# Optimization experiments

Measured on AMD Instinct MI355X. Metric: run time of the kernel, lower is better.

## Reference

```python
import jax, jax.numpy as jnp
import numpy as np

T, H, HS, NH = 1024, 2048, 64, 32
TM, TD = 32, 64  # time-mix / time-decay LoRA dims for hidden_size != 4096


def _layernorm(x, w, b, eps=1e-5):
    mu = jnp.mean(x, axis=-1, keepdims=True)
    var = jnp.mean(jnp.square(x - mu), axis=-1, keepdims=True)
    return (x - mu) * jax.lax.rsqrt(var + eps) * w + b


def setup_inputs() -> dict:
    key = jax.random.key(0)
    ks = jax.random.split(key, 16)
    s = 0.02
    return {
        'x': jax.random.normal(ks[0], (1, T, H), jnp.float32),
        'state1': jax.random.normal(ks[1], (1, H), jnp.float32),
        'state2': jax.random.normal(ks[2], (NH, HS, HS), jnp.float32) * s,
        'ln1_w': jnp.ones((H,), jnp.float32),
        'ln1_b': jnp.zeros((H,), jnp.float32),
        'time_maa_x': jax.random.normal(ks[3], (1, 1, H), jnp.float32) * s,
        'time_maa': jax.random.normal(ks[4], (5, 1, H), jnp.float32) * s,
        'time_maa_w1': jax.random.normal(ks[5], (H, 5 * TM), jnp.float32) * s,
        'time_maa_w2': jax.random.normal(ks[6], (5, TM, H), jnp.float32) * s,
        'time_decay_w1': jax.random.normal(ks[7], (H, TD), jnp.float32) * s,
        'time_decay_w2': jax.random.normal(ks[8], (TD, H), jnp.float32) * s,
        'time_decay_p': jax.random.normal(ks[9], (NH, 1, HS), jnp.float32),
        'time_first': jax.random.normal(ks[10], (NH, 1, HS), jnp.float32) * s,
        'W_r': jax.random.normal(ks[11], (H, H), jnp.float32) * s,
        'W_k': jax.random.normal(ks[12], (H, H), jnp.float32) * s,
        'W_v': jax.random.normal(ks[13], (H, H), jnp.float32) * s,
        'W_g': jax.random.normal(ks[14], (H, H), jnp.float32) * s,
        'W_o': jax.random.normal(ks[15], (H, H), jnp.float32) * s,
        'ln_x_w': jnp.ones((H,), jnp.float32),
        'ln_x_b': jnp.zeros((H,), jnp.float32),
    }


def _forward(x, state1, state2, ln1_w, ln1_b, time_maa_x, time_maa,
             time_maa_w1, time_maa_w2, time_decay_w1, time_decay_w2,
             time_decay_p, time_first, W_r, W_k, W_v, W_g, W_o, ln_x_w, ln_x_b):
    last_x = x
    xl = _layernorm(x, ln1_w, ln1_b)                 # (1,T,H)
    Tn = xl.shape[1]
    # token shift: sx = shift(x) - x, with state1 as the t=-1 token
    past = jnp.concatenate([state1[:, None, :], xl[:, :-1, :]], axis=1)
    sx = past - xl                                    # (1,T,H)
    state1_out = xl[:, -1, :]
    # data-dependent time-mix (LoRA through w1/w2)
    xxx = xl + sx * time_maa_x                        # (1,T,H)
    t5 = jnp.tanh(xxx[0] @ time_maa_w1)               # (T,5*TM)
    t5 = t5.reshape(Tn, 5, TM).transpose(1, 0, 2)     # (5,T,TM)
    mix = jnp.einsum('ftm,fmh->fth', t5, time_maa_w2) # (5,T,H)
    x5 = xl + sx * (mix + time_maa)                   # (5,T,H)
    mw, mk, mv, mr, mg = x5[0], x5[1], x5[2], x5[3], x5[4]
    r = (mr @ W_r).reshape(Tn, NH, HS)
    k = (mk @ W_k).reshape(Tn, NH, HS)
    v = (mv @ W_v).reshape(Tn, NH, HS)
    g = jax.nn.silu(mg @ W_g)                         # (T,H)
    # data-dependent decay
    td = (jnp.tanh(mw @ time_decay_w1) @ time_decay_w2).reshape(Tn, NH, 1, HS)
    td = td + time_decay_p                            # (T,NH,1,HS)
    td = jnp.exp(-jnp.exp(jnp.clip(td, -9.72, 2.27)))
    # WKV linear-attention recurrence
    kv = jnp.einsum('thi,thj->thij', v, k)            # (T,NH,HS,HS)

    def step(s2, inp):
        kv_t, r_t, td_t = inp
        tmp = kv_t * time_first + s2                  # (NH,HS,HS)
        wkv_t = jnp.einsum('hij,hj->hi', tmp, r_t)    # (NH,HS)
        return kv_t + s2 * td_t, wkv_t

    state2_out, wkv = jax.lax.scan(step, state2, (kv, r, td))  # wkv (T,NH,HS)
    # group-norm over head dim, then affine with ln_x params at hidden width
    y = _layernorm(wkv, 1.0, 0.0).reshape(1, Tn, H)
    y = (y * ln_x_w + ln_x_b) * g[None]
    y = y @ W_o
    return last_x + y, state1_out, state2_out


def reference(x, state1, state2, ln1_w, ln1_b, time_maa_x, time_maa,
              time_maa_w1, time_maa_w2, time_decay_w1, time_decay_w2,
              time_decay_p, time_first, W_r, W_k, W_v, W_g, W_o, ln_x_w, ln_x_b):
    return _forward(x, state1, state2, ln1_w, ln1_b, time_maa_x, time_maa,
                    time_maa_w1, time_maa_w2, time_decay_w1, time_decay_w2,
                    time_decay_p, time_first, W_r, W_k, W_v, W_g, W_o, ln_x_w, ln_x_b)
```

## Files before the change

kernel.cpp:

```cpp
#include <hip/hip_runtime.h>
#include <hip/hip_bf16.h>
#include <math.h>

#define TLEN 1024
#define HDIM 2048
#define NHEAD 32
#define HSZ 64
#define THE (TLEN * HDIM)
#define NC 32
#define CT (TLEN / NC)

typedef __attribute__((ext_vector_type(8))) short bf16x8;
typedef __attribute__((ext_vector_type(4))) float f32x4;

__device__ __forceinline__ float waveRedSum(float v) {
#pragma unroll
  for (int off = 32; off > 0; off >>= 1) v += __shfl_xor(v, off, 64);
  return v;
}

__device__ __forceinline__ void gll16(const __hip_bfloat16* g, __hip_bfloat16* l) {
  __builtin_amdgcn_global_load_lds(
      (const __attribute__((address_space(1))) void*)g,
      (__attribute__((address_space(3))) void*)l, 16, 0, 0);
}

struct TrArgs {
  const float* src[8];
  __hip_bfloat16* dst[8];
  int R[8];
  int C[8];
};

__global__ __launch_bounds__(256) void transp_kernel(TrArgs ta) {
  const int z = blockIdx.z;
  const int R = ta.R[z], C = ta.C[z];
  const int c0 = blockIdx.x * 32, r0 = blockIdx.y * 32;
  if (c0 >= C || r0 >= R) return;
  __shared__ float tile[32][33];
  const int tx = threadIdx.x & 31, ty = threadIdx.x >> 5;
  const float* src = ta.src[z];
  __hip_bfloat16* dst = ta.dst[z];
#pragma unroll
  for (int i = 0; i < 4; i++)
    tile[ty + i * 8][tx] = src[(size_t)(r0 + ty + i * 8) * C + c0 + tx];
  __syncthreads();
#pragma unroll
  for (int i = 0; i < 4; i++)
    dst[(size_t)(c0 + ty + i * 8) * R + r0 + tx] = __float2bfloat16(tile[tx][ty + i * 8]);
}

__global__ __launch_bounds__(256) void ln1_kernel(const float* __restrict__ x,
                                                  const float* __restrict__ w,
                                                  const float* __restrict__ b,
                                                  float* __restrict__ xl,
                                                  float* __restrict__ s1out) {
  const int t = blockIdx.x;
  const int tid = threadIdx.x;
  const int wid = tid >> 6, lane = tid & 63;
  const float4* xr = (const float4*)(x + (size_t)t * HDIM);
  float4 a = xr[tid];
  float4 c = xr[tid + 256];
  float va[8] = {a.x, a.y, a.z, a.w, c.x, c.y, c.z, c.w};
  float sum = 0.f;
#pragma unroll
  for (int i = 0; i < 8; i++) sum += va[i];
  sum = waveRedSum(sum);
  __shared__ float red[8];
  if (lane == 0) red[wid] = sum;
  __syncthreads();
  const float mu = (red[0] + red[1] + red[2] + red[3]) * (1.f / HDIM);
  float vs = 0.f;
#pragma unroll
  for (int i = 0; i < 8; i++) { float d = va[i] - mu; vs += d * d; }
  vs = waveRedSum(vs);
  if (lane == 0) red[4 + wid] = vs;
  __syncthreads();
  const float rstd = rsqrtf((red[4] + red[5] + red[6] + red[7]) * (1.f / HDIM) + 1e-5f);
  float* xrow = xl + (size_t)t * HDIM;
#pragma unroll
  for (int i = 0; i < 8; i++) {
    const int idx = (i < 4) ? (4 * tid + i) : (1024 + 4 * tid + (i - 4));
    const float o = (va[i] - mu) * rstd * w[idx] + b[idx];
    xrow[idx] = o;
    if (t == TLEN - 1) s1out[idx] = o;
  }
}

__global__ __launch_bounds__(256) void tokshift_kernel(const float* __restrict__ xl,
                                                       const float* __restrict__ s1,
                                                       const float* __restrict__ tmx,
                                                       __hip_bfloat16* __restrict__ xxx) {
  const int t = blockIdx.x;
  const int h = blockIdx.y * 256 + threadIdx.x;
  const float cur = xl[(size_t)t * HDIM + h];
  const float past = (t > 0) ? xl[(size_t)(t - 1) * HDIM + h] : s1[h];
  xxx[(size_t)t * HDIM + h] = __float2bfloat16(cur + (past - cur) * tmx[h]);
}

__global__ __launch_bounds__(256) void mix_kernel(const float* __restrict__ t5,
                                                  const float* __restrict__ xl,
                                                  const float* __restrict__ s1,
                                                  const float* __restrict__ w2,
                                                  const float* __restrict__ maa,
                                                  __hip_bfloat16* __restrict__ x5b) {
  const int h = blockIdx.x * 256 + threadIdx.x;
  const int t0 = blockIdx.y * 8;
  __shared__ float t5L[8 * 160];
  for (int i = threadIdx.x; i < 8 * 160; i += 256) {
    const int rr = i / 160, cc = i - rr * 160;
    t5L[i] = t5[(size_t)(t0 + rr) * 160 + cc];
  }
  __syncthreads();
  float mixv[8][5];
#pragma unroll
  for (int ts = 0; ts < 8; ts++)
#pragma unroll
    for (int f = 0; f < 5; f++) mixv[ts][f] = 0.f;
#pragma unroll
  for (int f = 0; f < 5; f++) {
#pragma unroll 4
    for (int m = 0; m < 32; m++) {
      const float w2v = w2[(size_t)(f * 32 + m) * HDIM + h];
#pragma unroll
      for (int ts = 0; ts < 8; ts++) mixv[ts][f] += t5L[ts * 160 + f * 32 + m] * w2v;
    }
  }
#pragma unroll
  for (int ts = 0; ts < 8; ts++) {
    const int t = t0 + ts;
    const float cur = xl[(size_t)t * HDIM + h];
    const float past = (t > 0) ? xl[(size_t)(t - 1) * HDIM + h] : s1[h];
    const float sx = past - cur;
#pragma unroll
    for (int f = 0; f < 5; f++) {
      const float v = cur + sx * (mixv[ts][f] + maa[(size_t)f * HDIM + h]);
      x5b[(size_t)f * THE + (size_t)t * HDIM + h] = __float2bfloat16(v);
    }
  }
}

struct GemmArgs {
  const __hip_bfloat16* A[8];
  const __hip_bfloat16* B[8];
  void* C[8];
  const float* aux[8];
  int epi[8];
  int M, N, K, Ks;
};

__global__ __launch_bounds__(256) void gemm_bt(GemmArgs ga) {
  const int z = blockIdx.z;
  const __hip_bfloat16* __restrict__ A = ga.A[z];
  const __hip_bfloat16* __restrict__ Bt = ga.B[z];
  const int N = ga.N, K = ga.K, Ks = ga.Ks;
  const int epi = ga.epi[z];
  const float* __restrict__ aux = ga.aux[z];
  void* Cz = ga.C[z];

  __shared__ __align__(16) __hip_bfloat16 As[2][128 * 64];
  __shared__ __align__(16) __hip_bfloat16 Bs[2][128 * 64];

  const int tid = threadIdx.x;
  const int wid = tid >> 6;
  const int lane = tid & 63;

  int bx = blockIdx.x, by = blockIdx.y;
  if (gridDim.x == 8 && gridDim.y == 16) {
    const int flat = bx + 8 * by;
    const int xcd = flat & 7, rem = flat >> 3;
    bx = rem & 7;
    by = xcd + 8 * (rem >> 3);
  }
  const int m0 = bx * 128;
  const int n0 = by * 128;
  const int wr = wid >> 1, wc = wid & 1;

  const int srow = lane >> 3;
  const int chunkS = (lane & 7) ^ srow;
  const __hip_bfloat16* aSrcQ[4];
  const __hip_bfloat16* bSrcQ[4];
#pragma unroll
  for (int q = 0; q < 4; q++) {
    const int arow = wid * 32 + q * 8 + srow;
    int brow = n0 + arow; if (brow > N - 1) brow = N - 1;
    aSrcQ[q] = A + (size_t)(m0 + arow) * Ks + chunkS * 8;
    bSrcQ[q] = Bt + (size_t)brow * Ks + chunkS * 8;
  }

  f32x4 acc[4][4];
#pragma unroll
  for (int m = 0; m < 4; m++)
#pragma unroll
    for (int n = 0; n < 4; n++) acc[m][n] = 0.f;

  const int lr = lane & 15;
  const int cbase = lane >> 4;
  int aoffk[2], boffk[2];
#pragma unroll
  for (int kg = 0; kg < 2; kg++) {
    const int phys = (kg * 4 + cbase) ^ (lr & 7);
    aoffk[kg] = (wr * 64 + lr) * 64 + phys * 8;
    boffk[kg] = (wc * 64 + lr) * 64 + phys * 8;
  }

#define STAGE(BUF, KT)                                              \
  do {                                                              \
    _Pragma("unroll") for (int q = 0; q < 4; q++) {                 \
      gll16(aSrcQ[q] + (KT), &As[BUF][(wid * 32 + q * 8) * 64]);    \
      gll16(bSrcQ[q] + (KT), &Bs[BUF][(wid * 32 + q * 8) * 64]);    \
    }                                                               \
  } while (0)

  STAGE(0, 0);
  int cur = 0;
  for (int kt = 0; kt < K; kt += 64) {
    const bool more = (kt + 64 < K);
    if (more) {
      STAGE(cur ^ 1, kt + 64);
      asm volatile("s_waitcnt vmcnt(8)" ::: "memory");
    } else {
      asm volatile("s_waitcnt vmcnt(0)" ::: "memory");
    }
    __builtin_amdgcn_s_barrier();
#pragma unroll
    for (int kg = 0; kg < 2; kg++) {
      bf16x8 af[4], bfv[4];
#pragma unroll
      for (int m = 0; m < 4; m++) af[m] = *(const bf16x8*)&As[cur][aoffk[kg] + m * 16 * 64];
#pragma unroll
      for (int n = 0; n < 4; n++) bfv[n] = *(const bf16x8*)&Bs[cur][boffk[kg] + n * 16 * 64];
#pragma unroll
      for (int m = 0; m < 4; m++)
#pragma unroll
        for (int n = 0; n < 4; n++)
          acc[m][n] = __builtin_amdgcn_mfma_f32_16x16x32_bf16(af[m], bfv[n], acc[m][n], 0, 0, 0);
    }
    __builtin_amdgcn_s_barrier();
    cur ^= 1;
  }
#undef STAGE

  const int r4 = (lane >> 4) * 4;
#pragma unroll
  for (int m = 0; m < 4; m++) {
#pragma unroll
    for (int n = 0; n < 4; n++) {
      const int gn = n0 + wc * 64 + n * 16 + lr;
      if (gn < N) {
#pragma unroll
        for (int r = 0; r < 4; r++) {
          const int gm = m0 + wr * 64 + m * 16 + r4 + r;
          const size_t idx = (size_t)gm * N + gn;
          const float v = acc[m][n][r];
          switch (epi) {
            case 0: ((__hip_bfloat16*)Cz)[idx] = __float2bfloat16(v); break;
            case 1: ((__hip_bfloat16*)Cz)[idx] = __float2bfloat16(v / (1.f + expf(-v))); break;
            case 2: ((float*)Cz)[idx] = tanhf(v); break;
            case 3: ((__hip_bfloat16*)Cz)[idx] = __float2bfloat16(tanhf(v)); break;
            case 5: ((float*)Cz)[idx] = v + aux[idx]; break;
            case 6: ((float*)Cz)[idx] = v; break;
          }
        }
      }
    }
  }
}

__global__ __launch_bounds__(256) void comb8_tanh_f32(const float* __restrict__ p,
                                                      float* __restrict__ o, int n) {
  const int i = blockIdx.x * 256 + threadIdx.x;
  float s = 0.f;
#pragma unroll
  for (int k = 0; k < 8; k++) s += p[(size_t)k * n + i];
  o[i] = tanhf(s);
}

__global__ __launch_bounds__(256) void comb8_tanh_bf16(const float* __restrict__ p,
                                                       __hip_bfloat16* __restrict__ o, int n) {
  const int i = blockIdx.x * 256 + threadIdx.x;
  float s = 0.f;
#pragma unroll
  for (int k = 0; k < 8; k++) s += p[(size_t)k * n + i];
  o[i] = __float2bfloat16(tanhf(s));
}

__global__ __launch_bounds__(256) void comb4_resid(const float* __restrict__ p,
                                                   const float* __restrict__ x,
                                                   float* __restrict__ o) {
  const int i = blockIdx.x * 256 + threadIdx.x;
  const float4 a = ((const float4*)p)[i];
  const float4 b = ((const float4*)(p + THE))[i];
  const float4 c = ((const float4*)(p + 2 * (size_t)THE))[i];
  const float4 d = ((const float4*)(p + 3 * (size_t)THE))[i];
  const float4 e = ((const float4*)x)[i];
  ((float4*)o)[i] = make_float4(a.x + b.x + c.x + d.x + e.x,
                                a.y + b.y + c.y + d.y + e.y,
                                a.z + b.z + c.z + d.z + e.z,
                                a.w + b.w + c.w + d.w + e.w);
}

__global__ __launch_bounds__(256) void tdcalc_kernel(const __hip_bfloat16* __restrict__ tw,
                                                     const __hip_bfloat16* __restrict__ dw2t,
                                                     const float* __restrict__ dp,
                                                     float* __restrict__ td) {
  const int t0 = blockIdx.x * 4;
  const int n = blockIdx.y * 256 + threadIdx.x;
  __shared__ float twL[4][64];
  {
    const int row = threadIdx.x >> 6, col = threadIdx.x & 63;
    twL[row][col] = __bfloat162float(tw[(size_t)(t0 + row) * 64 + col]);
  }
  __syncthreads();
  float acc[4] = {0.f, 0.f, 0.f, 0.f};
  const bf16x8* drow = (const bf16x8*)(dw2t + (size_t)n * 64);
#pragma unroll
  for (int ch = 0; ch < 8; ch++) {
    const bf16x8 v = drow[ch];
#pragma unroll
    for (int e = 0; e < 8; e++) {
      const float b = __builtin_bit_cast(float,
          (unsigned)((unsigned short)v[e]) << 16);
      const int col = ch * 8 + e;
#pragma unroll
      for (int r = 0; r < 4; r++) acc[r] = fmaf(twL[r][col], b, acc[r]);
    }
  }
  const float dpn = dp[n];
#pragma unroll
  for (int r = 0; r < 4; r++) {
    float wv = acc[r] + dpn;
    wv = fminf(fmaxf(wv, -9.72f), 2.27f);
    td[(size_t)(t0 + r) * HDIM + n] = expf(-expf(wv));
  }
}

__global__ __launch_bounds__(64) void decay_kernel(const __hip_bfloat16* __restrict__ rb,
                                                   const float* __restrict__ td,
                                                   __hip_bfloat16* __restrict__ rt,
                                                   float* __restrict__ Ptot) {
  const int blk = blockIdx.x;
  const int c = blk >> 5, h = blk & 31;
  const int j = threadIdx.x;
  const int hb = h * HSZ;
  const int t0 = c * CT;
  float A = 1.f;
  for (int t = 0; t < CT; t++) {
    const size_t rowb = (size_t)(t0 + t) * HDIM + hb;
    rt[(((size_t)c * NHEAD + h) * CT + t) * HSZ + j] =
        __float2bfloat16(__bfloat162float(rb[rowb + j]) * A);
    A *= td[rowb + j];
  }
  Ptot[((size_t)c * NHEAD + h) * HSZ + j] = A;
}

__global__ __launch_bounds__(256) void scan_local_kernel(const __hip_bfloat16* __restrict__ kb,
                                                         const __hip_bfloat16* __restrict__ rb,
                                                         const float* __restrict__ td,
                                                         const __hip_bfloat16* __restrict__ vb,
                                                         float* __restrict__ wkv,
                                                         float* __restrict__ qT) {
  const int blk = blockIdx.x;
  const int c = blk >> 5, h = blk & 31;
  const int w = threadIdx.x >> 6;
  const int i = threadIdx.x & 63;
  __shared__ float plds[2][4][64];

  float s[16];
#pragma unroll
  for (int q = 0; q < 16; q++) s[q] = 0.f;

  const int t0 = c * CT;
  const int hb = h * HSZ;

  for (int t = 0; t < CT; t++) {
    const size_t rowb = (size_t)(t0 + t) * HDIM + hb;
    const unsigned* kw = (const unsigned*)(kb + rowb + w * 16);
    const unsigned* rw = (const unsigned*)(rb + rowb + w * 16);
    const float* tdw = td + rowb + w * 16;
    const float vi = __bfloat162float(vb[rowb + i]);
    float p = 0.f;
#pragma unroll
    for (int m = 0; m < 8; m++) {
      const unsigned kpair = kw[m];
      const unsigned rpair = rw[m];
      const float k0 = __builtin_bit_cast(float, kpair << 16);
      const float k1 = __builtin_bit_cast(float, kpair & 0xffff0000u);
      const float r0 = __builtin_bit_cast(float, rpair << 16);
      const float r1 = __builtin_bit_cast(float, rpair & 0xffff0000u);
      const float td0 = tdw[2 * m];
      const float td1 = tdw[2 * m + 1];
      const float kv0 = vi * k0;
      const float kv1 = vi * k1;
      p = fmaf(r0, s[2 * m], p);
      p = fmaf(r1, s[2 * m + 1], p);
      s[2 * m] = fmaf(s[2 * m], td0, kv0);
      s[2 * m + 1] = fmaf(s[2 * m + 1], td1, kv1);
    }
    plds[t & 1][w][i] = p;
    __syncthreads();
    if (w == 0) {
      wkv[rowb + i] = plds[t & 1][0][i] + plds[t & 1][1][i] +
                      plds[t & 1][2][i] + plds[t & 1][3][i];
    }
  }
  float* qbase = qT + (((size_t)c * NHEAD + h) * HSZ + w * 16) * HSZ + i;
#pragma unroll
  for (int q = 0; q < 16; q++) qbase[(size_t)q * HSZ] = s[q];
}

__global__ __launch_bounds__(64) void scan_s_kernel(const float* __restrict__ qT,
                                                    const float* __restrict__ Ptot,
                                                    const float* __restrict__ s2in,
                                                    __hip_bfloat16* __restrict__ s0b,
                                                    float* __restrict__ s2out) {
  const int h = blockIdx.x, i = blockIdx.y, j = threadIdx.x;
  float s = s2in[((size_t)h * HSZ + i) * HSZ + j];
#pragma unroll 4
  for (int c = 0; c < NC; c++) {
    s0b[(((size_t)c * NHEAD + h) * HSZ + i) * HSZ + j] = __float2bfloat16(s);
    s = fmaf(s, Ptot[((size_t)c * NHEAD + h) * HSZ + j],
             qT[(((size_t)c * NHEAD + h) * HSZ + j) * HSZ + i]);
  }
  s2out[((size_t)h * HSZ + i) * HSZ + j] = s;
}

__global__ __launch_bounds__(256) void corr_kernel(const __hip_bfloat16* __restrict__ rt,
                                                   const __hip_bfloat16* __restrict__ s0b,
                                                   float* __restrict__ wkv) {
  const int c = blockIdx.x, h = blockIdx.y;
  const int w = threadIdx.x >> 6;
  const int lane = threadIdx.x & 63;
  const int lr = lane & 15, lk = (lane >> 4) * 8;
  const __hip_bfloat16* rbase = rt + (((size_t)c * NHEAD + h) * CT) * HSZ;
  const __hip_bfloat16* sbase = s0b + (((size_t)c * NHEAD + h) * HSZ) * HSZ;
  float* wbase = wkv + (size_t)(c * CT) * HDIM + h * HSZ;
#pragma unroll
  for (int mt = 0; mt < CT / 16; mt++) {
    f32x4 acc = {0.f, 0.f, 0.f, 0.f};
#pragma unroll
    for (int ks = 0; ks < 2; ks++) {
      bf16x8 af = *(const bf16x8*)(rbase + (size_t)(mt * 16 + lr) * HSZ + ks * 32 + lk);
      bf16x8 bf = *(const bf16x8*)(sbase + (size_t)(w * 16 + lr) * HSZ + ks * 32 + lk);
      acc = __builtin_amdgcn_mfma_f32_16x16x32_bf16(af, bf, acc, 0, 0, 0);
    }
    const int row = mt * 16 + (lane >> 4) * 4;
    const int col = w * 16 + lr;
#pragma unroll
    for (int r = 0; r < 4; r++)
      wbase[(size_t)(row + r) * HDIM + col] += acc[r];
  }
}

__global__ __launch_bounds__(256) void gnorm_kernel(const float* __restrict__ wkv,
                                                    const __hip_bfloat16* __restrict__ kb,
                                                    const __hip_bfloat16* __restrict__ rb,
                                                    const float* __restrict__ tf,
                                                    const __hip_bfloat16* __restrict__ vb,
                                                    const __hip_bfloat16* __restrict__ gb,
                                                    const float* __restrict__ lnw,
                                                    const float* __restrict__ lnb,
                                                    __hip_bfloat16* __restrict__ yA) {
  const int t = blockIdx.x;
  const int wid = threadIdx.x >> 6, j = threadIdx.x & 63;
  const int h = blockIdx.y * 4 + wid;
  const size_t idx = (size_t)t * HDIM + h * HSZ + j;
  const float kj = __bfloat162float(kb[idx]);
  const float rj = __bfloat162float(rb[idx]);
  const float dg = waveRedSum(rj * tf[h * HSZ + j] * kj);
  const float v = wkv[idx] + dg * __bfloat162float(vb[idx]);
  const float mu = waveRedSum(v) * (1.f / HSZ);
  const float d = v - mu;
  const float var = waveRedSum(d * d) * (1.f / HSZ);
  float y = d * rsqrtf(var + 1e-5f);
  y = y * lnw[h * HSZ + j] + lnb[h * HSZ + j];
  y *= __bfloat162float(gb[idx]);
  yA[idx] = __float2bfloat16(y);
}

extern "C" void kernel_launch(void* const* d_in, const int* in_sizes, int n_in,
                              void* d_out, int out_size, void* d_ws, size_t ws_size,
                              hipStream_t stream) {
  (void)in_sizes; (void)n_in; (void)out_size; (void)ws_size;

  const float* x    = (const float*)d_in[0];
  const float* s1   = (const float*)d_in[1];
  const float* s2   = (const float*)d_in[2];
  const float* ln1w = (const float*)d_in[3];
  const float* ln1b = (const float*)d_in[4];
  const float* tmx  = (const float*)d_in[5];
  const float* tmaa = (const float*)d_in[6];
  const float* w1   = (const float*)d_in[7];
  const float* w2   = (const float*)d_in[8];
  const float* dw1  = (const float*)d_in[9];
  const float* dw2  = (const float*)d_in[10];
  const float* dp   = (const float*)d_in[11];
  const float* tf   = (const float*)d_in[12];
  const float* Wr   = (const float*)d_in[13];
  const float* Wk   = (const float*)d_in[14];
  const float* Wv   = (const float*)d_in[15];
  const float* Wg   = (const float*)d_in[16];
  const float* Wo   = (const float*)d_in[17];
  const float* lnxw = (const float*)d_in[18];
  const float* lnxb = (const float*)d_in[19];

  float* out0  = (float*)d_out;
  float* s1out = out0 + (size_t)TLEN * HDIM;
  float* s2out = s1out + HDIM;

  char* wp = (char*)d_ws;
  size_t off = 0;
  auto carve = [&](size_t bytes) -> void* {
    void* r = wp + off;
    off += (bytes + 255) & ~(size_t)255;
    return r;
  };

  __hip_bfloat16* wrt  = (__hip_bfloat16*)carve((size_t)HDIM * HDIM * 2);
  __hip_bfloat16* wkt  = (__hip_bfloat16*)carve((size_t)HDIM * HDIM * 2);
  __hip_bfloat16* wvt  = (__hip_bfloat16*)carve((size_t)HDIM * HDIM * 2);
  __hip_bfloat16* wgt  = (__hip_bfloat16*)carve((size_t)HDIM * HDIM * 2);
  __hip_bfloat16* wot  = (__hip_bfloat16*)carve((size_t)HDIM * HDIM * 2);
  __hip_bfloat16* w1t  = (__hip_bfloat16*)carve((size_t)160 * HDIM * 2);
  __hip_bfloat16* dw1t = (__hip_bfloat16*)carve((size_t)64 * HDIM * 2);
  __hip_bfloat16* dw2t = (__hip_bfloat16*)carve((size_t)HDIM * 64 * 2);
  float* xl            = (float*)carve((size_t)THE * 4);
  __hip_bfloat16* xxx  = (__hip_bfloat16*)carve((size_t)THE * 2);
  float* t5            = (float*)carve((size_t)TLEN * 160 * 4);
  __hip_bfloat16* x5b  = (__hip_bfloat16*)carve((size_t)5 * THE * 2);
  __hip_bfloat16* rb   = (__hip_bfloat16*)carve((size_t)THE * 2);
  __hip_bfloat16* kb   = (__hip_bfloat16*)carve((size_t)THE * 2);
  __hip_bfloat16* vb   = (__hip_bfloat16*)carve((size_t)THE * 2);
  __hip_bfloat16* gb   = (__hip_bfloat16*)carve((size_t)THE * 2);
  __hip_bfloat16* tw   = (__hip_bfloat16*)carve((size_t)TLEN * 64 * 2);
  float* td            = (float*)carve((size_t)THE * 4);
  float* wkv           = (float*)carve((size_t)THE * 4);
  __hip_bfloat16* yA   = (__hip_bfloat16*)carve((size_t)THE * 2);

  float* qT            = (float*)x5b;
  __hip_bfloat16* rt   = (__hip_bfloat16*)xl;
  __hip_bfloat16* s0b  = (__hip_bfloat16*)td;
  float* Ptot          = (float*)t5;
  float* pg1           = (float*)td;
  float* pg4           = (float*)xxx;
  float* pg6           = (float*)x5b;

  TrArgs ta;
  const float* srcs[8] = {Wr, Wk, Wv, Wg, Wo, w1, dw1, dw2};
  __hip_bfloat16* dsts[8] = {wrt, wkt, wvt, wgt, wot, w1t, dw1t, dw2t};
  const int Rs[8] = {HDIM, HDIM, HDIM, HDIM, HDIM, HDIM, HDIM, 64};
  const int Cs[8] = {HDIM, HDIM, HDIM, HDIM, HDIM, 160, 64, HDIM};
  for (int z = 0; z < 8; z++) { ta.src[z] = srcs[z]; ta.dst[z] = dsts[z]; ta.R[z] = Rs[z]; ta.C[z] = Cs[z]; }
  transp_kernel<<<dim3(64, 64, 8), 256, 0, stream>>>(ta);

  ln1_kernel<<<dim3(TLEN), 256, 0, stream>>>(x, ln1w, ln1b, xl, s1out);

  tokshift_kernel<<<dim3(TLEN, HDIM / 256), 256, 0, stream>>>(xl, s1, tmx, xxx);

  {
    GemmArgs g{};
    for (int ks = 0; ks < 8; ks++) {
      g.A[ks] = xxx + ks * 256;
      g.B[ks] = w1t + ks * 256;
      g.C[ks] = pg1 + (size_t)ks * TLEN * 160;
      g.epi[ks] = 6;
    }
    g.M = TLEN; g.N = 160; g.K = 256; g.Ks = HDIM;
    gemm_bt<<<dim3(TLEN / 128, 2, 8), 256, 0, stream>>>(g);
    comb8_tanh_f32<<<dim3(TLEN * 160 / 256), 256, 0, stream>>>(pg1, t5, TLEN * 160);
  }

  mix_kernel<<<dim3(HDIM / 256, TLEN / 8), 256, 0, stream>>>(t5, xl, s1, w2, tmaa, x5b);

  {
    GemmArgs g{};
    g.A[0] = x5b + (size_t)3 * THE; g.B[0] = wrt; g.C[0] = rb; g.epi[0] = 0;
    g.A[1] = x5b + (size_t)1 * THE; g.B[1] = wkt; g.C[1] = kb; g.epi[1] = 0;
    g.A[2] = x5b + (size_t)2 * THE; g.B[2] = wvt; g.C[2] = vb; g.epi[2] = 0;
    g.A[3] = x5b + (size_t)4 * THE; g.B[3] = wgt; g.C[3] = gb; g.epi[3] = 1;
    g.M = TLEN; g.N = HDIM; g.K = HDIM; g.Ks = HDIM;
    gemm_bt<<<dim3(TLEN / 128, HDIM / 128, 4), 256, 0, stream>>>(g);
  }

  {
    GemmArgs g{};
    for (int ks = 0; ks < 8; ks++) {
      g.A[ks] = x5b + ks * 256;
      g.B[ks] = dw1t + ks * 256;
      g.C[ks] = pg4 + (size_t)ks * TLEN * 64;
      g.epi[ks] = 6;
    }
    g.M = TLEN; g.N = 64; g.K = 256; g.Ks = HDIM;
    gemm_bt<<<dim3(TLEN / 128, 1, 8), 256, 0, stream>>>(g);
    comb8_tanh_bf16<<<dim3(TLEN * 64 / 256), 256, 0, stream>>>(pg4, tw, TLEN * 64);
  }

  tdcalc_kernel<<<dim3(TLEN / 4, HDIM / 256), 256, 0, stream>>>(tw, dw2t, dp, td);

  decay_kernel<<<dim3(NC * NHEAD), 64, 0, stream>>>(rb, td, rt, Ptot);
  scan_local_kernel<<<dim3(NC * NHEAD), 256, 0, stream>>>(kb, rb, td, vb, wkv, qT);
  scan_s_kernel<<<dim3(NHEAD, HSZ), 64, 0, stream>>>(qT, Ptot, s2, s0b, s2out);
  corr_kernel<<<dim3(NC, NHEAD), 256, 0, stream>>>(rt, s0b, wkv);

  gnorm_kernel<<<dim3(TLEN, NHEAD / 4), 256, 0, stream>>>(wkv, kb, rb, tf, vb, gb, lnxw, lnxb, yA);

  {
    GemmArgs g{};
    for (int ks = 0; ks < 4; ks++) {
      g.A[ks] = yA + ks * 512;
      g.B[ks] = wot + ks * 512;
      g.C[ks] = pg6 + (size_t)ks * THE;
      g.epi[ks] = 6;
    }
    g.M = TLEN; g.N = HDIM; g.K = 512; g.Ks = HDIM;
    gemm_bt<<<dim3(TLEN / 128, HDIM / 128, 4), 256, 0, stream>>>(g);
    comb4_resid<<<dim3(THE / 4 / 256), 256, 0, stream>>>(pg6, x, out0);
  }
}
```

Measured before the change: 269.1 us.

## Fuse token-shift into LayerNorm, decay into local scan, and correction into group-norm

The token-shift kernel is removed: ln1 now normalizes both the current and previous row of x and writes the shifted bf16 mix directly. The decay-prefix kernel is folded into scan_local, which now also emits the decayed r values and the chunk's total decay. The MFMA correction kernel is replaced by a per-thread 64-element bf16 dot product inside gnorm. This cuts three launches and their intermediate round trips, at the cost of computing the previous row's LayerNorm twice and doing the correction with scalar FMAs instead of matrix instructions.

After: 312.9 us. 16.3% more time.

```diff
diff --git a/kernel.cpp b/kernel.cpp
--- a/kernel.cpp
+++ b/kernel.cpp
@@ -17,6 +17,10 @@
 #pragma unroll
   for (int off = 32; off > 0; off >>= 1) v += __shfl_xor(v, off, 64);
   return v;
+}
+
+__device__ __forceinline__ float bf2f(unsigned short u) {
+  return __builtin_bit_cast(float, (unsigned)u << 16);
 }
 
 __device__ __forceinline__ void gll16(const __hip_bfloat16* g, __hip_bfloat16* l) {
@@ -53,49 +57,54 @@
 __global__ __launch_bounds__(256) void ln1_kernel(const float* __restrict__ x,
                                                   const float* __restrict__ w,
                                                   const float* __restrict__ b,
+                                                  const float* __restrict__ s1,
+                                                  const float* __restrict__ tmx,
                                                   float* __restrict__ xl,
+                                                  __hip_bfloat16* __restrict__ xxx,
                                                   float* __restrict__ s1out) {
   const int t = blockIdx.x;
   const int tid = threadIdx.x;
   const int wid = tid >> 6, lane = tid & 63;
   const float4* xr = (const float4*)(x + (size_t)t * HDIM);
-  float4 a = xr[tid];
-  float4 c = xr[tid + 256];
+  const float4* xp = (const float4*)(x + (size_t)(t > 0 ? t - 1 : 0) * HDIM);
+  float4 a = xr[tid], c = xr[tid + 256];
+  float4 ap = xp[tid], cp = xp[tid + 256];
   float va[8] = {a.x, a.y, a.z, a.w, c.x, c.y, c.z, c.w};
-  float sum = 0.f;
-#pragma unroll
-  for (int i = 0; i < 8; i++) sum += va[i];
+  float vp[8] = {ap.x, ap.y, ap.z, ap.w, cp.x, cp.y, cp.z, cp.w};
+  float sum = 0.f, sump = 0.f;
+#pragma unroll
+  for (int i = 0; i < 8; i++) { sum += va[i]; sump += vp[i]; }
   sum = waveRedSum(sum);
-  __shared__ float red[8];
-  if (lane == 0) red[wid] = sum;
+  sump = waveRedSum(sump);
+  __shared__ float red[16];
+  if (lane == 0) { red[wid] = sum; red[8 + wid] = sump; }
   __syncthreads();
   const float mu = (red[0] + red[1] + red[2] + red[3]) * (1.f / HDIM);
-  float vs = 0.f;
-#pragma unroll
-  for (int i = 0; i < 8; i++) { float d = va[i] - mu; vs += d * d; }
+  const float mup = (red[8] + red[9] + red[10] + red[11]) * (1.f / HDIM);
+  float vs = 0.f, vsp = 0.f;
+#pragma unroll
+  for (int i = 0; i < 8; i++) {
+    float d = va[i] - mu; vs += d * d;
+    float dp = vp[i] - mup; vsp += dp * dp;
+  }
   vs = waveRedSum(vs);
-  if (lane == 0) red[4 + wid] = vs;
+  vsp = waveRedSum(vsp);
+  if (lane == 0) { red[4 + wid] = vs; red[12 + wid] = vsp; }
   __syncthreads();
   const float rstd = rsqrtf((red[4] + red[5] + red[6] + red[7]) * (1.f / HDIM) + 1e-5f);
+  const float rstdp = rsqrtf((red[12] + red[13] + red[14] + red[15]) * (1.f / HDIM) + 1e-5f);
   float* xrow = xl + (size_t)t * HDIM;
+  __hip_bfloat16* xxrow = xxx + (size_t)t * HDIM;
 #pragma unroll
   for (int i = 0; i < 8; i++) {
     const int idx = (i < 4) ? (4 * tid + i) : (1024 + 4 * tid + (i - 4));
-    const float o = (va[i] - mu) * rstd * w[idx] + b[idx];
-    xrow[idx] = o;
-    if (t == TLEN - 1) s1out[idx] = o;
-  }
-}
-
-__global__ __launch_bounds__(256) void tokshift_kernel(const float* __restrict__ xl,
-                                                       const float* __restrict__ s1,
-                                                       const float* __restrict__ tmx,
-                                                       __hip_bfloat16* __restrict__ xxx) {
-  const int t = blockIdx.x;
-  const int h = blockIdx.y * 256 + threadIdx.x;
-  const float cur = xl[(size_t)t * HDIM + h];
-  const float past = (t > 0) ? xl[(size_t)(t - 1) * HDIM + h] : s1[h];
-  xxx[(size_t)t * HDIM + h] = __float2bfloat16(cur + (past - cur) * tmx[h]);
+    const float wv = w[idx], bv = b[idx];
+    const float cur = (va[i] - mu) * rstd * wv + bv;
+    const float past = (t > 0) ? (vp[i] - mup) * rstdp * wv + bv : s1[idx];
+    xrow[idx] = cur;
+    xxrow[idx] = __float2bfloat16(cur + (past - cur) * tmx[idx]);
+    if (t == TLEN - 1) s1out[idx] = cur;
+  }
 }
 
 __global__ __launch_bounds__(256) void mix_kernel(const float* __restrict__ t5,
@@ -319,8 +328,7 @@
     const bf16x8 v = drow[ch];
 #pragma unroll
     for (int e = 0; e < 8; e++) {
-      const float b = __builtin_bit_cast(float,
-          (unsigned)((unsigned short)v[e]) << 16);
+      const float b = bf2f((unsigned short)v[e]);
       const int col = ch * 8 + e;
 #pragma unroll
       for (int r = 0; r < 4; r++) acc[r] = fmaf(twL[r][col], b, acc[r]);
@@ -333,25 +341,6 @@
     wv = fminf(fmaxf(wv, -9.72f), 2.27f);
     td[(size_t)(t0 + r) * HDIM + n] = expf(-expf(wv));
   }
-}
-
-__global__ __launch_bounds__(64) void decay_kernel(const __hip_bfloat16* __restrict__ rb,
-                                                   const float* __restrict__ td,
-                                                   __hip_bfloat16* __restrict__ rt,
-                                                   float* __restrict__ Ptot) {
-  const int blk = blockIdx.x;
-  const int c = blk >> 5, h = blk & 31;
-  const int j = threadIdx.x;
-  const int hb = h * HSZ;
-  const int t0 = c * CT;
-  float A = 1.f;
-  for (int t = 0; t < CT; t++) {
-    const size_t rowb = (size_t)(t0 + t) * HDIM + hb;
-    rt[(((size_t)c * NHEAD + h) * CT + t) * HSZ + j] =
-        __float2bfloat16(__bfloat162float(rb[rowb + j]) * A);
-    A *= td[rowb + j];
-  }
-  Ptot[((size_t)c * NHEAD + h) * HSZ + j] = A;
 }
 
 __global__ __launch_bounds__(256) void scan_local_kernel(const __hip_bfloat16* __restrict__ kb,
@@ -359,7 +348,9 @@
                                                          const float* __restrict__ td,
                                                          const __hip_bfloat16* __restrict__ vb,
                                                          float* __restrict__ wkv,
-                                                         float* __restrict__ qT) {
+                                                         float* __restrict__ qT,
+                                                         __hip_bfloat16* __restrict__ rt,
+                                                         float* __restrict__ Ptot) {
   const int blk = blockIdx.x;
   const int c = blk >> 5, h = blk & 31;
   const int w = threadIdx.x >> 6;
@@ -372,6 +363,9 @@
 
   const int t0 = c * CT;
   const int hb = h * HSZ;
+  const int jSelf = w * 16 + (i & 15);
+  float Aself = 1.f;
+  __hip_bfloat16* rtbase = rt + (((size_t)c * NHEAD + h) * CT) * HSZ + jSelf;
 
   for (int t = 0; t < CT; t++) {
     const size_t rowb = (size_t)(t0 + t) * HDIM + hb;
@@ -397,6 +391,10 @@
       s[2 * m] = fmaf(s[2 * m], td0, kv0);
       s[2 * m + 1] = fmaf(s[2 * m + 1], td1, kv1);
     }
+    const float rself = __bfloat162float(rb[rowb + jSelf]);
+    if (i < 16) rtbase[(size_t)t * HSZ] = __float2bfloat16(rself * Aself);
+    Aself *= td[rowb + jSelf];
+
     plds[t & 1][w][i] = p;
     __syncthreads();
     if (w == 0) {
@@ -404,6 +402,7 @@
                       plds[t & 1][2][i] + plds[t & 1][3][i];
     }
   }
+  if (i < 16) Ptot[((size_t)c * NHEAD + h) * HSZ + jSelf] = Aself;
   float* qbase = qT + (((size_t)c * NHEAD + h) * HSZ + w * 16) * HSZ + i;
 #pragma unroll
   for (int q = 0; q < 16; q++) qbase[(size_t)q * HSZ] = s[q];
@@ -425,39 +424,14 @@
   s2out[((size_t)h * HSZ + i) * HSZ + j] = s;
 }
 
-__global__ __launch_bounds__(256) void corr_kernel(const __hip_bfloat16* __restrict__ rt,
-                                                   const __hip_bfloat16* __restrict__ s0b,
-                                                   float* __restrict__ wkv) {
-  const int c = blockIdx.x, h = blockIdx.y;
-  const int w = threadIdx.x >> 6;
-  const int lane = threadIdx.x & 63;
-  const int lr = lane & 15, lk = (lane >> 4) * 8;
-  const __hip_bfloat16* rbase = rt + (((size_t)c * NHEAD + h) * CT) * HSZ;
-  const __hip_bfloat16* sbase = s0b + (((size_t)c * NHEAD + h) * HSZ) * HSZ;
-  float* wbase = wkv + (size_t)(c * CT) * HDIM + h * HSZ;
-#pragma unroll
-  for (int mt = 0; mt < CT / 16; mt++) {
-    f32x4 acc = {0.f, 0.f, 0.f, 0.f};
-#pragma unroll
-    for (int ks = 0; ks < 2; ks++) {
-      bf16x8 af = *(const bf16x8*)(rbase + (size_t)(mt * 16 + lr) * HSZ + ks * 32 + lk);
-      bf16x8 bf = *(const bf16x8*)(sbase + (size_t)(w * 16 + lr) * HSZ + ks * 32 + lk);
-      acc = __builtin_amdgcn_mfma_f32_16x16x32_bf16(af, bf, acc, 0, 0, 0);
-    }
-    const int row = mt * 16 + (lane >> 4) * 4;
-    const int col = w * 16 + lr;
-#pragma unroll
-    for (int r = 0; r < 4; r++)
-      wbase[(size_t)(row + r) * HDIM + col] += acc[r];
-  }
-}
-
 __global__ __launch_bounds__(256) void gnorm_kernel(const float* __restrict__ wkv,
                                                     const __hip_bfloat16* __restrict__ kb,
                                                     const __hip_bfloat16* __restrict__ rb,
                                                     const float* __restrict__ tf,
                                                     const __hip_bfloat16* __restrict__ vb,
                                                     const __hip_bfloat16* __restrict__ gb,
+                                                    const __hip_bfloat16* __restrict__ rt,
+                                                    const __hip_bfloat16* __restrict__ s0b,
                                                     const float* __restrict__ lnw,
                                                     const float* __restrict__ lnb,
                                                     __hip_bfloat16* __restrict__ yA) {
@@ -465,10 +439,24 @@
   const int wid = threadIdx.x >> 6, j = threadIdx.x & 63;
   const int h = blockIdx.y * 4 + wid;
   const size_t idx = (size_t)t * HDIM + h * HSZ + j;
+  const int c = t >> 5, tc = t & 31;
+
+  const bf16x8* rtrow = (const bf16x8*)(rt + (((size_t)c * NHEAD + h) * CT + tc) * HSZ);
+  const bf16x8* srow = (const bf16x8*)(s0b + (((size_t)c * NHEAD + h) * HSZ + j) * HSZ);
+  float corr = 0.f;
+#pragma unroll
+  for (int ch = 0; ch < 8; ch++) {
+    const bf16x8 rv = rtrow[ch];
+    const bf16x8 sv = srow[ch];
+#pragma unroll
+    for (int e = 0; e < 8; e++)
+      corr = fmaf(bf2f((unsigned short)rv[e]), bf2f((unsigned short)sv[e]), corr);
+  }
+
   const float kj = __bfloat162float(kb[idx]);
   const float rj = __bfloat162float(rb[idx]);
   const float dg = waveRedSum(rj * tf[h * HSZ + j] * kj);
-  const float v = wkv[idx] + dg * __bfloat162float(vb[idx]);
+  const float v = wkv[idx] + corr + dg * __bfloat162float(vb[idx]);
   const float mu = waveRedSum(v) * (1.f / HSZ);
   const float d = v - mu;
   const float var = waveRedSum(d * d) * (1.f / HSZ);
@@ -553,9 +541,7 @@
   for (int z = 0; z < 8; z++) { ta.src[z] = srcs[z]; ta.dst[z] = dsts[z]; ta.R[z] = Rs[z]; ta.C[z] = Cs[z]; }
   transp_kernel<<<dim3(64, 64, 8), 256, 0, stream>>>(ta);
 
-  ln1_kernel<<<dim3(TLEN), 256, 0, stream>>>(x, ln1w, ln1b, xl, s1out);
-
-  tokshift_kernel<<<dim3(TLEN, HDIM / 256), 256, 0, stream>>>(xl, s1, tmx, xxx);
+  ln1_kernel<<<dim3(TLEN), 256, 0, stream>>>(x, ln1w, ln1b, s1, tmx, xl, xxx, s1out);
 
   {
     GemmArgs g{};
@@ -597,12 +583,11 @@
 
   tdcalc_kernel<<<dim3(TLEN / 4, HDIM / 256), 256, 0, stream>>>(tw, dw2t, dp, td);
 
-  decay_kernel<<<dim3(NC * NHEAD), 64, 0, stream>>>(rb, td, rt, Ptot);
-  scan_local_kernel<<<dim3(NC * NHEAD), 256, 0, stream>>>(kb, rb, td, vb, wkv, qT);
+  scan_local_kernel<<<dim3(NC * NHEAD), 256, 0, stream>>>(kb, rb, td, vb, wkv, qT, rt, Ptot);
   scan_s_kernel<<<dim3(NHEAD, HSZ), 64, 0, stream>>>(qT, Ptot, s2, s0b, s2out);
-  corr_kernel<<<dim3(NC, NHEAD), 256, 0, stream>>>(rt, s0b, wkv);
-
-  gnorm_kernel<<<dim3(TLEN, NHEAD / 4), 256, 0, stream>>>(wkv, kb, rb, tf, vb, gb, lnxw, lnxb, yA);
+
+  gnorm_kernel<<<dim3(TLEN, NHEAD / 4), 256, 0, stream>>>(wkv, kb, rb, tf, vb, gb, rt, s0b,
+                                                          lnxw, lnxb, yA);
 
   {
     GemmArgs g{};
```
